# Kernel optimization log

Hardware: AMD Instinct MI355X
Metric: run time of the kernel (lower is better)

Reference implementation:

```python
import jax, jax.numpy as jnp
import numpy as np

STEPS = 3


def setup_inputs() -> dict:
    key = jax.random.key(0)
    ks = jax.random.split(key, 6)
    N, H, B = 1000000, 128, 16384
    x = jax.random.normal(ks[0], (N, H), dtype=jnp.float32)
    batch_vec = jnp.sort(jax.random.randint(ks[1], (N,), 0, B)).astype(jnp.int64)
    scale_ih = 1.0 / np.sqrt(2 * H)
    scale_hh = 1.0 / np.sqrt(H)
    W_ih = jax.random.normal(ks[2], (4 * H, 2 * H), dtype=jnp.float32) * scale_ih
    W_hh = jax.random.normal(ks[3], (4 * H, H), dtype=jnp.float32) * scale_hh
    b_ih = jnp.zeros((4 * H,), dtype=jnp.float32)
    b_hh = jnp.zeros((4 * H,), dtype=jnp.float32)
    return {"x": x, "batch_vec": batch_vec, "W_ih": W_ih, "W_hh": W_hh,
            "b_ih": b_ih, "b_hh": b_hh, "num_graphs": B}


def _set2set(x, batch_vec, W_ih, W_hh, b_ih, b_hh, B):
    N, H = x.shape
    q_star = jnp.zeros((B, 2 * H), x.dtype)
    h = jnp.zeros((B, H), x.dtype)
    c = jnp.zeros((B, H), x.dtype)
    bias = b_ih + b_hh
    for _ in range(STEPS):
        # LSTMCell (torch gate order: i, f, g, o)
        gates = q_star @ W_ih.T + h @ W_hh.T + bias  # [B, 4H]
        i, f, g, o = jnp.split(gates, 4, axis=-1)
        c = jax.nn.sigmoid(f) * c + jax.nn.sigmoid(i) * jnp.tanh(g)
        h = jax.nn.sigmoid(o) * jnp.tanh(c)
        q = h  # [B, H]
        # attention logits per node
        e = jnp.sum(x * q[batch_vec], axis=-1)  # [N]
        emax = jax.ops.segment_max(e, batch_vec, num_segments=B)
        emax = jax.lax.stop_gradient(jnp.where(jnp.isfinite(emax), emax, 0.0))
        ex = jnp.exp(e - emax[batch_vec])
        denom = jax.ops.segment_sum(ex, batch_vec, num_segments=B)
        a = ex / denom[batch_vec]  # segment softmax, [N]
        r = jax.ops.segment_sum(a[:, None] * x, batch_vec, num_segments=B)  # [B, H]
        q_star = jnp.concatenate([q, r], axis=-1)  # [B, 2H]
    return q_star


def reference(x, batch_vec, W_ih, W_hh, b_ih, b_hh, num_graphs):
    return _set2set(x, batch_vec, W_ih, W_hh, b_ih, b_hh, int(num_graphs))
```

## Files before the change

### kernel.cpp

```cpp
#include <hip/hip_runtime.h>
#include <math.h>

#define HDIM 128
#define G4 512
#define TS 36

typedef float vf4 __attribute__((ext_vector_type(4)));
typedef unsigned short u16x8 __attribute__((ext_vector_type(8)));

__device__ __forceinline__ float sigm(float v) { return 1.0f / (1.0f + __expf(-v)); }
__device__ __forceinline__ float ftanh(float v) {
    return 1.0f - 2.0f / (__expf(2.0f * v) + 1.0f);
}
__device__ __forceinline__ float dot4(vf4 a, vf4 b) {
    return a.x * b.x + a.y * b.y + a.z * b.z + a.w * b.w;
}
__device__ __forceinline__ vf4 ldnt4(const float* p) {
    return __builtin_nontemporal_load((const vf4*)p);
}
__device__ __forceinline__ unsigned short f2bf(float f) {
    unsigned u = __float_as_uint(f);
    u += 0x7fff + ((u >> 16) & 1);
    return (unsigned short)(u >> 16);
}
__device__ __forceinline__ float bf2f(unsigned short h) {
    return __uint_as_float(((unsigned)h) << 16);
}

__global__ __launch_bounds__(256) void k_setup(const float* __restrict__ W_ih,
                                               const float* __restrict__ W_hh,
                                               const float* __restrict__ b_ih,
                                               const float* __restrict__ b_hh,
                                               const int* __restrict__ batch_vec, int N, int B,
                                               float* __restrict__ Wc, int* __restrict__ seg_start,
                                               float* __restrict__ h, float* __restrict__ c) {
    int t = blockIdx.x * 256 + threadIdx.x;
    if (t < B * HDIM) {
        int hid = t & (HDIM - 1);
        float gi = b_ih[hid] + b_hh[hid];
        float gg = b_ih[2 * HDIM + hid] + b_hh[2 * HDIM + hid];
        float go = b_ih[3 * HDIM + hid] + b_hh[3 * HDIM + hid];
        float cv = sigm(gi) * ftanh(gg);
        c[t] = cv;
        h[t] = sigm(go) * ftanh(cv);
    }
    if (t < G4 * 2 * HDIM) {
        int g = t >> 8;
        int k = t & 255;
        float w = W_ih[g * 256 + k];
        if (k < HDIM) w += W_hh[g * HDIM + k];
        Wc[t] = w;
    }
    if (t <= B) {
        int lo = 0, hi = N;
        while (lo < hi) {
            int mid = (lo + hi) >> 1;
            if (batch_vec[mid] < t) lo = mid + 1; else hi = mid;
        }
        seg_start[t] = lo;
    }
}

#define UPD(m_, d_, ra_, rb_, p_, xa_, xb_)  \
    {                                        \
        float mn_ = fmaxf(m_, p_);           \
        float sc_ = __expf(m_ - mn_);        \
        float pe_ = __expf(p_ - mn_);        \
        d_ = d_ * sc_ + pe_;                 \
        ra_ = ra_ * sc_ + pe_ * xa_;         \
        rb_ = rb_ * sc_ + pe_ * xb_;         \
        m_ = mn_;                            \
    }

#define MERGE_AND_WRITE()                                                     \
    {                                                                         \
        float M = fmaxf(m0, m1);                                              \
        float w0 = __expf(m0 - M), w1 = __expf(m1 - M);                       \
        d0 = d0 * w0 + d1 * w1;                                               \
        ra0 = ra0 * w0 + ra1 * w1;                                            \
        rb0 = rb0 * w0 + rb1 * w1;                                            \
        m0 = M;                                                               \
    }                                                                         \
    _Pragma("unroll")                                                         \
    for (int off = 16; off <= 32; off <<= 1) {                                \
        float om = __shfl_xor(m0, off, 64);                                   \
        float M = fmaxf(m0, om);                                              \
        float w = __expf(m0 - M);                                             \
        d0 *= w; ra0 *= w; rb0 *= w;                                          \
        d0 += __shfl_xor(d0, off, 64);                                        \
        ra0.x += __shfl_xor(ra0.x, off, 64);                                  \
        ra0.y += __shfl_xor(ra0.y, off, 64);                                  \
        ra0.z += __shfl_xor(ra0.z, off, 64);                                  \
        ra0.w += __shfl_xor(ra0.w, off, 64);                                  \
        rb0.x += __shfl_xor(rb0.x, off, 64);                                  \
        rb0.y += __shfl_xor(rb0.y, off, 64);                                  \
        rb0.z += __shfl_xor(rb0.z, off, 64);                                  \
        rb0.w += __shfl_xor(rb0.w, off, 64);                                  \
        m0 = M;                                                               \
    }                                                                         \
    float inv = (d0 > 0.0f) ? 1.0f / d0 : 0.0f;                               \
    if (quarter == 0) {                                                       \
        float* dst = r_out + (size_t)seg * ldr + col_off + l16 * 8;           \
        *(vf4*)dst = ra0 * inv;                                               \
        *(vf4*)(dst + 4) = rb0 * inv;                                         \
    }

__global__ __launch_bounds__(256) void k_attn_cvt(const float* __restrict__ x,
                                                  unsigned short* __restrict__ x16,
                                                  const float* __restrict__ q,
                                                  const int* __restrict__ seg_start,
                                                  float* __restrict__ r_out, int B) {
    const int ldr = HDIM, col_off = 0;
    int wave = threadIdx.x >> 6;
    int lane = threadIdx.x & 63;
    int l16 = lane & 15;
    int quarter = lane >> 4;
    int seg = (blockIdx.x << 2) + wave;
    if (seg >= B) return;
    int s = seg_start[seg], e = seg_start[seg + 1];

    const float* qrow = q + (size_t)seg * HDIM + l16 * 8;
    vf4 qa = *(const vf4*)qrow;
    vf4 qb = *(const vf4*)(qrow + 4);

    float m0 = 0.0f, d0 = 0.0f, m1 = 0.0f, d1 = 0.0f;
    vf4 ra0 = {0.f, 0.f, 0.f, 0.f}, rb0 = {0.f, 0.f, 0.f, 0.f};
    vf4 ra1 = {0.f, 0.f, 0.f, 0.f}, rb1 = {0.f, 0.f, 0.f, 0.f};

    int base = s;
#pragma unroll 2
    for (; base + 8 <= e; base += 8) {
        const float* xr0 = x + (size_t)(base + quarter) * HDIM + l16 * 8;
        const float* xr1 = xr0 + 4 * HDIM;
        vf4 xa0 = ldnt4(xr0), xb0 = ldnt4(xr0 + 4);
        vf4 xa1 = ldnt4(xr1), xb1 = ldnt4(xr1 + 4);
        u16x8 c0, c1;
        c0[0] = f2bf(xa0.x); c0[1] = f2bf(xa0.y); c0[2] = f2bf(xa0.z); c0[3] = f2bf(xa0.w);
        c0[4] = f2bf(xb0.x); c0[5] = f2bf(xb0.y); c0[6] = f2bf(xb0.z); c0[7] = f2bf(xb0.w);
        c1[0] = f2bf(xa1.x); c1[1] = f2bf(xa1.y); c1[2] = f2bf(xa1.z); c1[3] = f2bf(xa1.w);
        c1[4] = f2bf(xb1.x); c1[5] = f2bf(xb1.y); c1[6] = f2bf(xb1.z); c1[7] = f2bf(xb1.w);
        *(u16x8*)(x16 + (size_t)(base + quarter) * HDIM + l16 * 8) = c0;
        *(u16x8*)(x16 + (size_t)(base + 4 + quarter) * HDIM + l16 * 8) = c1;
        float p0 = dot4(xa0, qa) + dot4(xb0, qb);
        float p1 = dot4(xa1, qa) + dot4(xb1, qb);
        p0 += __shfl_xor(p0, 1, 64);  p1 += __shfl_xor(p1, 1, 64);
        p0 += __shfl_xor(p0, 2, 64);  p1 += __shfl_xor(p1, 2, 64);
        p0 += __shfl_xor(p0, 4, 64);  p1 += __shfl_xor(p1, 4, 64);
        p0 += __shfl_xor(p0, 8, 64);  p1 += __shfl_xor(p1, 8, 64);
        UPD(m0, d0, ra0, rb0, p0, xa0, xb0)
        UPD(m1, d1, ra1, rb1, p1, xa1, xb1)
    }
    for (; base < e; base += 4) {
        int row = base + quarter;
        const float* xr = x + (size_t)min(row, e - 1) * HDIM + l16 * 8;
        vf4 xa = ldnt4(xr), xb = ldnt4(xr + 4);
        u16x8 c0;
        c0[0] = f2bf(xa.x); c0[1] = f2bf(xa.y); c0[2] = f2bf(xa.z); c0[3] = f2bf(xa.w);
        c0[4] = f2bf(xb.x); c0[5] = f2bf(xb.y); c0[6] = f2bf(xb.z); c0[7] = f2bf(xb.w);
        *(u16x8*)(x16 + (size_t)min(row, e - 1) * HDIM + l16 * 8) = c0;
        float p = dot4(xa, qa) + dot4(xb, qb);
        p += __shfl_xor(p, 1, 64);
        p += __shfl_xor(p, 2, 64);
        p += __shfl_xor(p, 4, 64);
        p += __shfl_xor(p, 8, 64);
        if (row >= e) p = -1e30f;
        UPD(m0, d0, ra0, rb0, p, xa, xb)
    }
    MERGE_AND_WRITE()
}

__global__ __launch_bounds__(256) void k_attn_b16(const unsigned short* __restrict__ x16,
                                                  const float* __restrict__ q,
                                                  const int* __restrict__ seg_start,
                                                  float* __restrict__ r_out, int ldr, int col_off,
                                                  int B, int rev) {
    int wave = threadIdx.x >> 6;
    int lane = threadIdx.x & 63;
    int l16 = lane & 15;
    int quarter = lane >> 4;
    int gid = (blockIdx.x << 2) + wave;
    if (gid >= B) return;
    int seg = rev ? (B - 1 - gid) : gid;
    int s = seg_start[seg], e = seg_start[seg + 1];

    const float* qrow = q + (size_t)seg * HDIM + l16 * 8;
    vf4 qa = *(const vf4*)qrow;
    vf4 qb = *(const vf4*)(qrow + 4);

    float m0 = 0.0f, d0 = 0.0f, m1 = 0.0f, d1 = 0.0f;
    vf4 ra0 = {0.f, 0.f, 0.f, 0.f}, rb0 = {0.f, 0.f, 0.f, 0.f};
    vf4 ra1 = {0.f, 0.f, 0.f, 0.f}, rb1 = {0.f, 0.f, 0.f, 0.f};

    int base = s;
#pragma unroll 2
    for (; base + 8 <= e; base += 8) {
        const unsigned short* xr0 = x16 + (size_t)(base + quarter) * HDIM + l16 * 8;
        u16x8 u0 = *(const u16x8*)xr0;
        u16x8 u1 = *(const u16x8*)(xr0 + 4 * HDIM);
        vf4 xa0 = {bf2f(u0[0]), bf2f(u0[1]), bf2f(u0[2]), bf2f(u0[3])};
        vf4 xb0 = {bf2f(u0[4]), bf2f(u0[5]), bf2f(u0[6]), bf2f(u0[7])};
        vf4 xa1 = {bf2f(u1[0]), bf2f(u1[1]), bf2f(u1[2]), bf2f(u1[3])};
        vf4 xb1 = {bf2f(u1[4]), bf2f(u1[5]), bf2f(u1[6]), bf2f(u1[7])};
        float p0 = dot4(xa0, qa) + dot4(xb0, qb);
        float p1 = dot4(xa1, qa) + dot4(xb1, qb);
        p0 += __shfl_xor(p0, 1, 64);  p1 += __shfl_xor(p1, 1, 64);
        p0 += __shfl_xor(p0, 2, 64);  p1 += __shfl_xor(p1, 2, 64);
        p0 += __shfl_xor(p0, 4, 64);  p1 += __shfl_xor(p1, 4, 64);
        p0 += __shfl_xor(p0, 8, 64);  p1 += __shfl_xor(p1, 8, 64);
        UPD(m0, d0, ra0, rb0, p0, xa0, xb0)
        UPD(m1, d1, ra1, rb1, p1, xa1, xb1)
    }
    for (; base < e; base += 4) {
        int row = base + quarter;
        const unsigned short* xr = x16 + (size_t)min(row, e - 1) * HDIM + l16 * 8;
        u16x8 u0 = *(const u16x8*)xr;
        vf4 xa = {bf2f(u0[0]), bf2f(u0[1]), bf2f(u0[2]), bf2f(u0[3])};
        vf4 xb = {bf2f(u0[4]), bf2f(u0[5]), bf2f(u0[6]), bf2f(u0[7])};
        float p = dot4(xa, qa) + dot4(xb, qb);
        p += __shfl_xor(p, 1, 64);
        p += __shfl_xor(p, 2, 64);
        p += __shfl_xor(p, 4, 64);
        p += __shfl_xor(p, 8, 64);
        if (row >= e) p = -1e30f;
        UPD(m0, d0, ra0, rb0, p, xa, xb)
    }
    MERGE_AND_WRITE()
}

__global__ __launch_bounds__(256) void k_gemm_lstm(const float* __restrict__ h_prev,
                                                   const float* __restrict__ r_prev,
                                                   const float* __restrict__ c_prev,
                                                   const float* __restrict__ Wc,
                                                   const float* __restrict__ b_ih,
                                                   const float* __restrict__ b_hh,
                                                   float* __restrict__ h_new,
                                                   float* __restrict__ c_new,
                                                   float* __restrict__ h_mirror) {
    __shared__ float As[128 * TS];
    __shared__ float Ws[64 * TS];
    int ct = blockIdx.y;
    int rb = blockIdx.x * 128;
    int tid = threadIdx.x;
    int tx = tid & 15, ty = tid >> 4;
    float acc[8][4];
#pragma unroll
    for (int i = 0; i < 8; ++i)
#pragma unroll
        for (int j = 0; j < 4; ++j) acc[i][j] = 0.0f;

    for (int kc = 0; kc < 8; ++kc) {
        const float* src = (kc < 4) ? h_prev : r_prev;
        int kbase = (kc & 3) * 32;
#pragma unroll
        for (int i = 0; i < 4; ++i) {
            int li = tid + i * 256;
            int row = li >> 3;
            int c4 = (li & 7) * 4;
            *(vf4*)&As[row * TS + c4] = *(const vf4*)(src + (size_t)(rb + row) * HDIM + kbase + c4);
        }
#pragma unroll
        for (int i = 0; i < 2; ++i) {
            int li = tid + i * 256;
            int col = li >> 3;
            int c4 = (li & 7) * 4;
            int g = ct * 16 + (col & 15) + 128 * (col >> 4);
            *(vf4*)&Ws[col * TS + c4] = *(const vf4*)(Wc + (size_t)g * 256 + kc * 32 + c4);
        }
        __syncthreads();
#pragma unroll
        for (int k = 0; k < 32; k += 4) {
            vf4 a[8], b[4];
#pragma unroll
            for (int i = 0; i < 8; ++i) a[i] = *(vf4*)&As[(ty + 16 * i) * TS + k];
#pragma unroll
            for (int j = 0; j < 4; ++j) b[j] = *(vf4*)&Ws[(tx + 16 * j) * TS + k];
#pragma unroll
            for (int i = 0; i < 8; ++i)
#pragma unroll
                for (int j = 0; j < 4; ++j) {
                    acc[i][j] += a[i].x * b[j].x + a[i].y * b[j].y +
                                 a[i].z * b[j].z + a[i].w * b[j].w;
                }
        }
        __syncthreads();
    }
    int hidx = ct * 16 + tx;
    float bi = b_ih[hidx] + b_hh[hidx];
    float bf = b_ih[HDIM + hidx] + b_hh[HDIM + hidx];
    float bg = b_ih[2 * HDIM + hidx] + b_hh[2 * HDIM + hidx];
    float bo = b_ih[3 * HDIM + hidx] + b_hh[3 * HDIM + hidx];
#pragma unroll
    for (int i = 0; i < 8; ++i) {
        int row = rb + ty + 16 * i;
        float gi = acc[i][0] + bi;
        float gf = acc[i][1] + bf;
        float gg = acc[i][2] + bg;
        float go = acc[i][3] + bo;
        float cp = c_prev[(size_t)row * HDIM + hidx];
        float cn = sigm(gf) * cp + sigm(gi) * ftanh(gg);
        float hn = sigm(go) * ftanh(cn);
        c_new[(size_t)row * HDIM + hidx] = cn;
        h_new[(size_t)row * HDIM + hidx] = hn;
        if (h_mirror) h_mirror[(size_t)row * 2 * HDIM + hidx] = hn;
    }
}

extern "C" void kernel_launch(void* const* d_in, const int* in_sizes, int n_in,
                              void* d_out, int out_size, void* d_ws, size_t ws_size,
                              hipStream_t stream) {
    const float* x = (const float*)d_in[0];
    const int* batch_vec = (const int*)d_in[1];
    const float* W_ih = (const float*)d_in[2];
    const float* W_hh = (const float*)d_in[3];
    const float* b_ih = (const float*)d_in[4];
    const float* b_hh = (const float*)d_in[5];
    float* out = (float*)d_out;

    int N = in_sizes[1];
    int B = out_size / (2 * HDIM);

    char* ws = (char*)d_ws;
    float* Wc = (float*)ws;            ws += (size_t)G4 * 2 * HDIM * 4;
    float* h_a = (float*)ws;           ws += (size_t)B * HDIM * 4;
    float* h_b = (float*)ws;           ws += (size_t)B * HDIM * 4;
    float* cbuf = (float*)ws;          ws += (size_t)B * HDIM * 4;
    float* rbuf = (float*)ws;          ws += (size_t)B * HDIM * 4;
    int* seg = (int*)ws;               ws += (size_t)(B + 1) * 4;
    ws = (char*)(((size_t)ws + 255) & ~(size_t)255);
    unsigned short* x16 = (unsigned short*)ws;

    int setup_grid = (B * HDIM + 255) / 256;
    k_setup<<<setup_grid, 256, 0, stream>>>(W_ih, W_hh, b_ih, b_hh, batch_vec, N, B,
                                            Wc, seg, h_a, cbuf);

    dim3 ggrid(B / 128, 8);
    k_attn_cvt<<<(B + 3) / 4, 256, 0, stream>>>(x, x16, h_a, seg, rbuf, B);
    k_gemm_lstm<<<ggrid, 256, 0, stream>>>(h_a, rbuf, cbuf, Wc, b_ih, b_hh, h_b, cbuf, nullptr);
    k_attn_b16<<<(B + 3) / 4, 256, 0, stream>>>(x16, h_b, seg, rbuf, HDIM, 0, B, 1);
    k_gemm_lstm<<<ggrid, 256, 0, stream>>>(h_b, rbuf, cbuf, Wc, b_ih, b_hh, h_a, cbuf, out);
    k_attn_b16<<<(B + 3) / 4, 256, 0, stream>>>(x16, h_a, seg, out, 2 * HDIM, HDIM, B, 0);
}
```

Before: 487.7 us.

## Specialize first LSTM step using constant initial hidden state and widen attention unroll

The first LSTM state is identical for every graph because q_star and h start at zero. The change therefore computes it once from the biases instead of materialising per-graph h and c buffers in setup. A new k_head kernel precomputes the W_hh·h0 contribution into gh0. The second gate GEMM then only multiplies the r half (K=128) in a dedicated k_gemm_lstm1 kernel, which halves its work and its reads. Separately, the attention loops now process 16 rows per iteration with all loads issued up front, for more memory-level parallelism at the cost of extra registers.

Result: no change. 478.9 us (-1.8%).

```diff
diff --git a/kernel.cpp b/kernel.cpp
--- a/kernel.cpp
+++ b/kernel.cpp
@@ -29,21 +29,9 @@
 
 __global__ __launch_bounds__(256) void k_setup(const float* __restrict__ W_ih,
                                                const float* __restrict__ W_hh,
-                                               const float* __restrict__ b_ih,
-                                               const float* __restrict__ b_hh,
                                                const int* __restrict__ batch_vec, int N, int B,
-                                               float* __restrict__ Wc, int* __restrict__ seg_start,
-                                               float* __restrict__ h, float* __restrict__ c) {
+                                               float* __restrict__ Wc, int* __restrict__ seg_start) {
     int t = blockIdx.x * 256 + threadIdx.x;
-    if (t < B * HDIM) {
-        int hid = t & (HDIM - 1);
-        float gi = b_ih[hid] + b_hh[hid];
-        float gg = b_ih[2 * HDIM + hid] + b_hh[2 * HDIM + hid];
-        float go = b_ih[3 * HDIM + hid] + b_hh[3 * HDIM + hid];
-        float cv = sigm(gi) * ftanh(gg);
-        c[t] = cv;
-        h[t] = sigm(go) * ftanh(cv);
-    }
     if (t < G4 * 2 * HDIM) {
         int g = t >> 8;
         int k = t & 255;
@@ -59,6 +47,30 @@
         }
         seg_start[t] = lo;
     }
+}
+
+__global__ __launch_bounds__(256) void k_head(const float* __restrict__ Wc,
+                                              const float* __restrict__ b_ih,
+                                              const float* __restrict__ b_hh,
+                                              float* __restrict__ gh0) {
+    __shared__ float h0s[HDIM];
+    int t = threadIdx.x;
+    int g = blockIdx.x * 256 + t;
+    if (t < HDIM) {
+        float bi = b_ih[t] + b_hh[t];
+        float bg = b_ih[2 * HDIM + t] + b_hh[2 * HDIM + t];
+        float bo = b_ih[3 * HDIM + t] + b_hh[3 * HDIM + t];
+        float c0 = sigm(bi) * ftanh(bg);
+        h0s[t] = sigm(bo) * ftanh(c0);
+    }
+    __syncthreads();
+    float s = 0.0f;
+#pragma unroll
+    for (int k = 0; k < HDIM; k += 4) {
+        vf4 w = *(const vf4*)(Wc + (size_t)g * 256 + k);
+        s += w.x * h0s[k] + w.y * h0s[k + 1] + w.z * h0s[k + 2] + w.w * h0s[k + 3];
+    }
+    gh0[g] = s;
 }
 
 #define UPD(m_, d_, ra_, rb_, p_, xa_, xb_)  \
@@ -71,6 +83,12 @@
         rb_ = rb_ * sc_ + pe_ * xb_;         \
         m_ = mn_;                            \
     }
+
+#define SHFL16(p_)                  \
+    p_ += __shfl_xor(p_, 1, 64);    \
+    p_ += __shfl_xor(p_, 2, 64);    \
+    p_ += __shfl_xor(p_, 4, 64);    \
+    p_ += __shfl_xor(p_, 8, 64);
 
 #define MERGE_AND_WRITE()                                                     \
     {                                                                         \
@@ -107,7 +125,8 @@
 
 __global__ __launch_bounds__(256) void k_attn_cvt(const float* __restrict__ x,
                                                   unsigned short* __restrict__ x16,
-                                                  const float* __restrict__ q,
+                                                  const float* __restrict__ b_ih,
+                                                  const float* __restrict__ b_hh,
                                                   const int* __restrict__ seg_start,
                                                   float* __restrict__ r_out, int B) {
     const int ldr = HDIM, col_off = 0;
@@ -119,50 +138,65 @@
     if (seg >= B) return;
     int s = seg_start[seg], e = seg_start[seg + 1];
 
-    const float* qrow = q + (size_t)seg * HDIM + l16 * 8;
-    vf4 qa = *(const vf4*)qrow;
-    vf4 qb = *(const vf4*)(qrow + 4);
+    vf4 qa, qb;
+    {
+        int c = l16 * 8;
+        vf4 bi0 = *(const vf4*)(b_ih + c) + *(const vf4*)(b_hh + c);
+        vf4 bi1 = *(const vf4*)(b_ih + c + 4) + *(const vf4*)(b_hh + c + 4);
+        vf4 bg0 = *(const vf4*)(b_ih + 2 * HDIM + c) + *(const vf4*)(b_hh + 2 * HDIM + c);
+        vf4 bg1 = *(const vf4*)(b_ih + 2 * HDIM + c + 4) + *(const vf4*)(b_hh + 2 * HDIM + c + 4);
+        vf4 bo0 = *(const vf4*)(b_ih + 3 * HDIM + c) + *(const vf4*)(b_hh + 3 * HDIM + c);
+        vf4 bo1 = *(const vf4*)(b_ih + 3 * HDIM + c + 4) + *(const vf4*)(b_hh + 3 * HDIM + c + 4);
+#pragma unroll
+        for (int j = 0; j < 4; ++j) {
+            float c0 = sigm(bi0[j]) * ftanh(bg0[j]);
+            qa[j] = sigm(bo0[j]) * ftanh(c0);
+            float c1 = sigm(bi1[j]) * ftanh(bg1[j]);
+            qb[j] = sigm(bo1[j]) * ftanh(c1);
+        }
+    }
 
     float m0 = 0.0f, d0 = 0.0f, m1 = 0.0f, d1 = 0.0f;
     vf4 ra0 = {0.f, 0.f, 0.f, 0.f}, rb0 = {0.f, 0.f, 0.f, 0.f};
     vf4 ra1 = {0.f, 0.f, 0.f, 0.f}, rb1 = {0.f, 0.f, 0.f, 0.f};
 
     int base = s;
-#pragma unroll 2
-    for (; base + 8 <= e; base += 8) {
-        const float* xr0 = x + (size_t)(base + quarter) * HDIM + l16 * 8;
-        const float* xr1 = xr0 + 4 * HDIM;
-        vf4 xa0 = ldnt4(xr0), xb0 = ldnt4(xr0 + 4);
-        vf4 xa1 = ldnt4(xr1), xb1 = ldnt4(xr1 + 4);
-        u16x8 c0, c1;
-        c0[0] = f2bf(xa0.x); c0[1] = f2bf(xa0.y); c0[2] = f2bf(xa0.z); c0[3] = f2bf(xa0.w);
-        c0[4] = f2bf(xb0.x); c0[5] = f2bf(xb0.y); c0[6] = f2bf(xb0.z); c0[7] = f2bf(xb0.w);
-        c1[0] = f2bf(xa1.x); c1[1] = f2bf(xa1.y); c1[2] = f2bf(xa1.z); c1[3] = f2bf(xa1.w);
-        c1[4] = f2bf(xb1.x); c1[5] = f2bf(xb1.y); c1[6] = f2bf(xb1.z); c1[7] = f2bf(xb1.w);
-        *(u16x8*)(x16 + (size_t)(base + quarter) * HDIM + l16 * 8) = c0;
-        *(u16x8*)(x16 + (size_t)(base + 4 + quarter) * HDIM + l16 * 8) = c1;
-        float p0 = dot4(xa0, qa) + dot4(xb0, qb);
-        float p1 = dot4(xa1, qa) + dot4(xb1, qb);
-        p0 += __shfl_xor(p0, 1, 64);  p1 += __shfl_xor(p1, 1, 64);
-        p0 += __shfl_xor(p0, 2, 64);  p1 += __shfl_xor(p1, 2, 64);
-        p0 += __shfl_xor(p0, 4, 64);  p1 += __shfl_xor(p1, 4, 64);
-        p0 += __shfl_xor(p0, 8, 64);  p1 += __shfl_xor(p1, 8, 64);
-        UPD(m0, d0, ra0, rb0, p0, xa0, xb0)
-        UPD(m1, d1, ra1, rb1, p1, xa1, xb1)
-    }
+#pragma unroll 1
+    for (; base + 16 <= e; base += 16) {
+        vf4 xa[4], xb[4];
+        float p[4];
+#pragma unroll
+        for (int t = 0; t < 4; ++t) {
+            const float* xr = x + (size_t)(base + quarter + 4 * t) * HDIM + l16 * 8;
+            xa[t] = ldnt4(xr);
+            xb[t] = ldnt4(xr + 4);
+        }
+#pragma unroll
+        for (int t = 0; t < 4; ++t) {
+            u16x8 cv;
+            cv[0] = f2bf(xa[t].x); cv[1] = f2bf(xa[t].y); cv[2] = f2bf(xa[t].z); cv[3] = f2bf(xa[t].w);
+            cv[4] = f2bf(xb[t].x); cv[5] = f2bf(xb[t].y); cv[6] = f2bf(xb[t].z); cv[7] = f2bf(xb[t].w);
+            *(u16x8*)(x16 + (size_t)(base + quarter + 4 * t) * HDIM + l16 * 8) = cv;
+            p[t] = dot4(xa[t], qa) + dot4(xb[t], qb);
+        }
+        SHFL16(p[0]) SHFL16(p[1]) SHFL16(p[2]) SHFL16(p[3])
+        UPD(m0, d0, ra0, rb0, p[0], xa[0], xb[0])
+        UPD(m1, d1, ra1, rb1, p[1], xa[1], xb[1])
+        UPD(m0, d0, ra0, rb0, p[2], xa[2], xb[2])
+        UPD(m1, d1, ra1, rb1, p[3], xa[3], xb[3])
+    }
+#pragma unroll 1
     for (; base < e; base += 4) {
         int row = base + quarter;
-        const float* xr = x + (size_t)min(row, e - 1) * HDIM + l16 * 8;
+        int rl = min(row, e - 1);
+        const float* xr = x + (size_t)rl * HDIM + l16 * 8;
         vf4 xa = ldnt4(xr), xb = ldnt4(xr + 4);
-        u16x8 c0;
-        c0[0] = f2bf(xa.x); c0[1] = f2bf(xa.y); c0[2] = f2bf(xa.z); c0[3] = f2bf(xa.w);
-        c0[4] = f2bf(xb.x); c0[5] = f2bf(xb.y); c0[6] = f2bf(xb.z); c0[7] = f2bf(xb.w);
-        *(u16x8*)(x16 + (size_t)min(row, e - 1) * HDIM + l16 * 8) = c0;
+        u16x8 cv;
+        cv[0] = f2bf(xa.x); cv[1] = f2bf(xa.y); cv[2] = f2bf(xa.z); cv[3] = f2bf(xa.w);
+        cv[4] = f2bf(xb.x); cv[5] = f2bf(xb.y); cv[6] = f2bf(xb.z); cv[7] = f2bf(xb.w);
+        *(u16x8*)(x16 + (size_t)rl * HDIM + l16 * 8) = cv;
         float p = dot4(xa, qa) + dot4(xb, qb);
-        p += __shfl_xor(p, 1, 64);
-        p += __shfl_xor(p, 2, 64);
-        p += __shfl_xor(p, 4, 64);
-        p += __shfl_xor(p, 8, 64);
+        SHFL16(p)
         if (row >= e) p = -1e30f;
         UPD(m0, d0, ra0, rb0, p, xa, xb)
     }
@@ -192,39 +226,114 @@
     vf4 ra1 = {0.f, 0.f, 0.f, 0.f}, rb1 = {0.f, 0.f, 0.f, 0.f};
 
     int base = s;
-#pragma unroll 2
-    for (; base + 8 <= e; base += 8) {
-        const unsigned short* xr0 = x16 + (size_t)(base + quarter) * HDIM + l16 * 8;
-        u16x8 u0 = *(const u16x8*)xr0;
-        u16x8 u1 = *(const u16x8*)(xr0 + 4 * HDIM);
-        vf4 xa0 = {bf2f(u0[0]), bf2f(u0[1]), bf2f(u0[2]), bf2f(u0[3])};
-        vf4 xb0 = {bf2f(u0[4]), bf2f(u0[5]), bf2f(u0[6]), bf2f(u0[7])};
-        vf4 xa1 = {bf2f(u1[0]), bf2f(u1[1]), bf2f(u1[2]), bf2f(u1[3])};
-        vf4 xb1 = {bf2f(u1[4]), bf2f(u1[5]), bf2f(u1[6]), bf2f(u1[7])};
-        float p0 = dot4(xa0, qa) + dot4(xb0, qb);
-        float p1 = dot4(xa1, qa) + dot4(xb1, qb);
-        p0 += __shfl_xor(p0, 1, 64);  p1 += __shfl_xor(p1, 1, 64);
-        p0 += __shfl_xor(p0, 2, 64);  p1 += __shfl_xor(p1, 2, 64);
-        p0 += __shfl_xor(p0, 4, 64);  p1 += __shfl_xor(p1, 4, 64);
-        p0 += __shfl_xor(p0, 8, 64);  p1 += __shfl_xor(p1, 8, 64);
-        UPD(m0, d0, ra0, rb0, p0, xa0, xb0)
-        UPD(m1, d1, ra1, rb1, p1, xa1, xb1)
-    }
+#pragma unroll 1
+    for (; base + 16 <= e; base += 16) {
+        vf4 xa[4], xb[4];
+        float p[4];
+#pragma unroll
+        for (int t = 0; t < 4; ++t) {
+            const unsigned short* xr = x16 + (size_t)(base + quarter + 4 * t) * HDIM + l16 * 8;
+            u16x8 u = *(const u16x8*)xr;
+            xa[t] = vf4{bf2f(u[0]), bf2f(u[1]), bf2f(u[2]), bf2f(u[3])};
+            xb[t] = vf4{bf2f(u[4]), bf2f(u[5]), bf2f(u[6]), bf2f(u[7])};
+        }
+#pragma unroll
+        for (int t = 0; t < 4; ++t) p[t] = dot4(xa[t], qa) + dot4(xb[t], qb);
+        SHFL16(p[0]) SHFL16(p[1]) SHFL16(p[2]) SHFL16(p[3])
+        UPD(m0, d0, ra0, rb0, p[0], xa[0], xb[0])
+        UPD(m1, d1, ra1, rb1, p[1], xa[1], xb[1])
+        UPD(m0, d0, ra0, rb0, p[2], xa[2], xb[2])
+        UPD(m1, d1, ra1, rb1, p[3], xa[3], xb[3])
+    }
+#pragma unroll 1
     for (; base < e; base += 4) {
         int row = base + quarter;
         const unsigned short* xr = x16 + (size_t)min(row, e - 1) * HDIM + l16 * 8;
-        u16x8 u0 = *(const u16x8*)xr;
-        vf4 xa = {bf2f(u0[0]), bf2f(u0[1]), bf2f(u0[2]), bf2f(u0[3])};
-        vf4 xb = {bf2f(u0[4]), bf2f(u0[5]), bf2f(u0[6]), bf2f(u0[7])};
+        u16x8 u = *(const u16x8*)xr;
+        vf4 xa = {bf2f(u[0]), bf2f(u[1]), bf2f(u[2]), bf2f(u[3])};
+        vf4 xb = {bf2f(u[4]), bf2f(u[5]), bf2f(u[6]), bf2f(u[7])};
         float p = dot4(xa, qa) + dot4(xb, qb);
-        p += __shfl_xor(p, 1, 64);
-        p += __shfl_xor(p, 2, 64);
-        p += __shfl_xor(p, 4, 64);
-        p += __shfl_xor(p, 8, 64);
+        SHFL16(p)
         if (row >= e) p = -1e30f;
         UPD(m0, d0, ra0, rb0, p, xa, xb)
     }
     MERGE_AND_WRITE()
+}
+
+__global__ __launch_bounds__(256) void k_gemm_lstm1(const float* __restrict__ r_prev,
+                                                    const float* __restrict__ Wc,
+                                                    const float* __restrict__ gh0,
+                                                    const float* __restrict__ b_ih,
+                                                    const float* __restrict__ b_hh,
+                                                    float* __restrict__ h_new,
+                                                    float* __restrict__ c_new) {
+    __shared__ float As[128 * TS];
+    __shared__ float Ws[64 * TS];
+    int ct = blockIdx.y;
+    int rb = blockIdx.x * 128;
+    int tid = threadIdx.x;
+    int tx = tid & 15, ty = tid >> 4;
+    float acc[8][4];
+#pragma unroll
+    for (int i = 0; i < 8; ++i)
+#pragma unroll
+        for (int j = 0; j < 4; ++j) acc[i][j] = 0.0f;
+
+    for (int kc = 0; kc < 4; ++kc) {
+        int kbase = kc * 32;
+#pragma unroll
+        for (int i = 0; i < 4; ++i) {
+            int li = tid + i * 256;
+            int row = li >> 3;
+            int c4 = (li & 7) * 4;
+            *(vf4*)&As[row * TS + c4] = *(const vf4*)(r_prev + (size_t)(rb + row) * HDIM + kbase + c4);
+        }
+#pragma unroll
+        for (int i = 0; i < 2; ++i) {
+            int li = tid + i * 256;
+            int col = li >> 3;
+            int c4 = (li & 7) * 4;
+            int g = ct * 16 + (col & 15) + 128 * (col >> 4);
+            *(vf4*)&Ws[col * TS + c4] = *(const vf4*)(Wc + (size_t)g * 256 + 128 + kbase + c4);
+        }
+        __syncthreads();
+#pragma unroll
+        for (int k = 0; k < 32; k += 4) {
+            vf4 a[8], b[4];
+#pragma unroll
+            for (int i = 0; i < 8; ++i) a[i] = *(vf4*)&As[(ty + 16 * i) * TS + k];
+#pragma unroll
+            for (int j = 0; j < 4; ++j) b[j] = *(vf4*)&Ws[(tx + 16 * j) * TS + k];
+#pragma unroll
+            for (int i = 0; i < 8; ++i)
+#pragma unroll
+                for (int j = 0; j < 4; ++j) {
+                    acc[i][j] += a[i].x * b[j].x + a[i].y * b[j].y +
+                                 a[i].z * b[j].z + a[i].w * b[j].w;
+                }
+        }
+        __syncthreads();
+    }
+    int hidx = ct * 16 + tx;
+    float bi = b_ih[hidx] + b_hh[hidx] + gh0[hidx];
+    float bf = b_ih[HDIM + hidx] + b_hh[HDIM + hidx] + gh0[HDIM + hidx];
+    float bg = b_ih[2 * HDIM + hidx] + b_hh[2 * HDIM + hidx] + gh0[2 * HDIM + hidx];
+    float bo = b_ih[3 * HDIM + hidx] + b_hh[3 * HDIM + hidx] + gh0[3 * HDIM + hidx];
+    float bi0 = b_ih[hidx] + b_hh[hidx];
+    float bg0 = b_ih[2 * HDIM + hidx] + b_hh[2 * HDIM + hidx];
+    float c0 = sigm(bi0) * ftanh(bg0);
+#pragma unroll
+    for (int i = 0; i < 8; ++i) {
+        int row = rb + ty + 16 * i;
+        float gi = acc[i][0] + bi;
+        float gf = acc[i][1] + bf;
+        float gg = acc[i][2] + bg;
+        float go = acc[i][3] + bo;
+        float cn = sigm(gf) * c0 + sigm(gi) * ftanh(gg);
+        float hn = sigm(go) * ftanh(cn);
+        c_new[(size_t)row * HDIM + hidx] = cn;
+        h_new[(size_t)row * HDIM + hidx] = hn;
+    }
 }
 
 __global__ __launch_bounds__(256) void k_gemm_lstm(const float* __restrict__ h_prev,
@@ -321,6 +430,7 @@
 
     char* ws = (char*)d_ws;
     float* Wc = (float*)ws;            ws += (size_t)G4 * 2 * HDIM * 4;
+    float* gh0 = (float*)ws;           ws += (size_t)G4 * 4;
     float* h_a = (float*)ws;           ws += (size_t)B * HDIM * 4;
     float* h_b = (float*)ws;           ws += (size_t)B * HDIM * 4;
     float* cbuf = (float*)ws;          ws += (size_t)B * HDIM * 4;
@@ -329,13 +439,12 @@
     ws = (char*)(((size_t)ws + 255) & ~(size_t)255);
     unsigned short* x16 = (unsigned short*)ws;
 
-    int setup_grid = (B * HDIM + 255) / 256;
-    k_setup<<<setup_grid, 256, 0, stream>>>(W_ih, W_hh, b_ih, b_hh, batch_vec, N, B,
-                                            Wc, seg, h_a, cbuf);
+    k_setup<<<512, 256, 0, stream>>>(W_ih, W_hh, batch_vec, N, B, Wc, seg);
+    k_head<<<2, 256, 0, stream>>>(Wc, b_ih, b_hh, gh0);
 
     dim3 ggrid(B / 128, 8);
-    k_attn_cvt<<<(B + 3) / 4, 256, 0, stream>>>(x, x16, h_a, seg, rbuf, B);
-    k_gemm_lstm<<<ggrid, 256, 0, stream>>>(h_a, rbuf, cbuf, Wc, b_ih, b_hh, h_b, cbuf, nullptr);
+    k_attn_cvt<<<(B + 3) / 4, 256, 0, stream>>>(x, x16, b_ih, b_hh, seg, rbuf, B);
+    k_gemm_lstm1<<<ggrid, 256, 0, stream>>>(rbuf, Wc, gh0, b_ih, b_hh, h_b, cbuf);
     k_attn_b16<<<(B + 3) / 4, 256, 0, stream>>>(x16, h_b, seg, rbuf, HDIM, 0, B, 1);
     k_gemm_lstm<<<ggrid, 256, 0, stream>>>(h_b, rbuf, cbuf, Wc, b_ih, b_hh, h_a, cbuf, out);
     k_attn_b16<<<(B + 3) / 4, 256, 0, stream>>>(x16, h_a, seg, out, 2 * HDIM, HDIM, B, 0);
```
